# Optimization experiments

Measured on AMD Instinct MI355X. Metric: run time of the kernel, lower is better.

## Reference

```python
import jax, jax.numpy as jnp
import numpy as np

N = 100000   # num entities / tail rows
D_IN = 128
D_OUT = 128
R = 8        # num relations
E = 131072   # edges per relation
B = 32768    # head entities per relation


def setup_inputs() -> dict:
    key = jax.random.key(0)
    ks = jax.random.split(key, 8)
    x = jax.random.normal(ks[0], (N, D_IN), dtype=jnp.float32)
    tail_rep = jax.random.normal(ks[1], (N, D_IN), dtype=jnp.float32)
    # Linear(in, out, bias=False) weight: [out, in], xavier-ish scale
    W = jax.random.normal(ks[2], (D_OUT, D_IN), dtype=jnp.float32) * (1.414 / np.sqrt(D_IN))
    # match_matrix embedding -> per-relation [in, out] matrices
    rel_W = jax.random.normal(ks[3], (R, D_IN, D_OUT), dtype=jnp.float32) * (1.0 / np.sqrt(D_IN))
    edge_weights = jax.random.uniform(ks[4], (R, E), dtype=jnp.float32)
    edge_rows = jax.random.randint(ks[5], (R, E), 0, B, dtype=jnp.int32)
    edge_cols = jax.random.randint(ks[6], (R, E), 0, N, dtype=jnp.int32)
    # head_indice: unique global entity ids per relation (torch code assigns by index)
    rng = np.random.default_rng(0)
    head = np.stack([rng.choice(N, size=B, replace=False) for _ in range(R)]).astype(np.int32)
    head_indice = jnp.asarray(head)
    return {"x": x, "tail_rep": tail_rep, "W": W, "rel_W": rel_W,
            "edge_weights": edge_weights, "edge_rows": edge_rows,
            "edge_cols": edge_cols, "head_indice": head_indice}


def reference(x, tail_rep, W, rel_W, edge_weights, edge_rows, edge_cols, head_indice):
    # emb_all = original_map(input)
    emb_all = x @ W.T                                   # [N, D_OUT]
    # per-relation dense transform of all tails: tail_rep @ rel_W[r]
    transformed = jnp.einsum('ni,rio->rno', tail_rep, rel_W)   # [R, N, D_OUT]
    # sparse.mm(sp_edge_e, all_rep_h): gather tail rows per edge, weight, segment-sum by local head row
    gathered = jnp.take_along_axis(transformed, edge_cols[:, :, None], axis=1)  # [R, E, D_OUT]
    contrib = edge_weights[:, :, None] * gathered                                # [R, E, D_OUT]
    seg = lambda c, rows: jax.ops.segment_sum(c, rows, num_segments=B)
    new_rep = jax.vmap(seg)(contrib, edge_rows)                                  # [R, B, D_OUT]
    # emb_all[ent_indice] = rel_update + emb_all[ent_indice]  (per relation, sequentially) == scatter-add
    emb_all = emb_all.at[head_indice.reshape(-1)].add(new_rep.reshape(-1, D_OUT))
    # activate=True
    return jax.nn.relu(emb_all)
```

## Files before the change

kernel.cpp:

```cpp
#include <hip/hip_runtime.h>
#include <hip/hip_bf16.h>

#define D_DIM 128
#define N_ENT 100000
#define R_REL 8
#define E_EDGE 131072
#define B_HEAD 32768
#define NH_PAD 100352

typedef __attribute__((ext_vector_type(8))) short short8v;
typedef __attribute__((ext_vector_type(16))) float f32x16;
typedef unsigned int uint;
typedef unsigned short ushort;

union BF8 {
  short8v v;
  __hip_bfloat16 h[8];
};

__device__ inline ushort bfbits(float x) {
  union { __hip_bfloat16 h; ushort u; } c;
  c.h = __float2bfloat16(x);
  return c.u;
}
__device__ inline float bflo(uint p) { return __uint_as_float(p << 16); }
__device__ inline float bfhi(uint p) { return __uint_as_float(p & 0xffff0000u); }

__global__ __launch_bounds__(256) void init_ws(int* __restrict__ cnt_e,
                                               int* __restrict__ inv) {
  int i = blockIdx.x * 256 + threadIdx.x;
  if (i < R_REL * B_HEAD) cnt_e[i] = 0;
  inv[i] = -1;
}

__global__ __launch_bounds__(256) void prep_bf16(const float* __restrict__ src,
                                                 short8v* __restrict__ dst) {
  int i = blockIdx.x * 256 + threadIdx.x;
  const float4* s = (const float4*)src + (size_t)i * 2;
  float4 a = s[0], b = s[1];
  BF8 h;
  h.h[0] = __float2bfloat16(a.x); h.h[1] = __float2bfloat16(a.y);
  h.h[2] = __float2bfloat16(a.z); h.h[3] = __float2bfloat16(a.w);
  h.h[4] = __float2bfloat16(b.x); h.h[5] = __float2bfloat16(b.y);
  h.h[6] = __float2bfloat16(b.z); h.h[7] = __float2bfloat16(b.w);
  dst[i] = h.v;
}

__global__ __launch_bounds__(256) void hist_edges(const int* __restrict__ erow,
                                                  int* __restrict__ cnt) {
  int r = blockIdx.y;
  int e = blockIdx.x * 256 + threadIdx.x;
  int row = erow[(size_t)r * E_EDGE + e];
  atomicAdd(cnt + r * B_HEAD + row, 1);
}

__global__ __launch_bounds__(256) void scan_blk(const int* __restrict__ cnt,
                                                int* __restrict__ cur,
                                                int* __restrict__ bsum) {
  int b = blockIdx.x, t = threadIdx.x;
  int4 v = ((const int4*)cnt)[b * 256 + t];
  int s = v.x + v.y + v.z + v.w;
  __shared__ int ps[256];
  ps[t] = s;
  __syncthreads();
  for (int off = 1; off < 256; off <<= 1) {
    int u = (t >= off) ? ps[t - off] : 0;
    __syncthreads();
    ps[t] += u;
    __syncthreads();
  }
  int base = ps[t] - s;
  int4 o;
  o.x = base; o.y = base + v.x; o.z = o.y + v.y; o.w = o.z + v.z;
  ((int4*)cur)[b * 256 + t] = o;
  if (t == 255) bsum[b] = ps[255];
}

__global__ __launch_bounds__(256) void scan_bsum(int* __restrict__ bsum) {
  int t = threadIdx.x;
  int s = bsum[t];
  __shared__ int ps[256];
  ps[t] = s;
  __syncthreads();
  for (int off = 1; off < 256; off <<= 1) {
    int u = (t >= off) ? ps[t - off] : 0;
    __syncthreads();
    ps[t] += u;
    __syncthreads();
  }
  bsum[t] = ps[t] - s;
}

__global__ __launch_bounds__(256) void scan_add(int* __restrict__ cur,
                                                const int* __restrict__ bsum) {
  int i = blockIdx.x * 256 + threadIdx.x;
  int o = bsum[i >> 8];
  int4 v = ((int4*)cur)[i];
  v.x += o; v.y += o; v.z += o; v.w += o;
  ((int4*)cur)[i] = v;
}

__global__ __launch_bounds__(256) void scatter_edges(const int* __restrict__ erow,
                                                     const int* __restrict__ ecol,
                                                     const float* __restrict__ ew,
                                                     int* __restrict__ cur,
                                                     int2* __restrict__ sColW) {
  int r = blockIdx.y;
  int e = blockIdx.x * 256 + threadIdx.x;
  size_t idx = (size_t)r * E_EDGE + e;
  int row = erow[idx];
  int pos = atomicAdd(cur + r * B_HEAD + row, 1);
  sColW[pos] = make_int2(ecol[idx], __float_as_int(ew[idx]));
}

__global__ __launch_bounds__(256) void build_inv(const int* __restrict__ head,
                                                 int* __restrict__ inv) {
  int i = blockIdx.x * 256 + threadIdx.x;
  int r = i >> 15;
  inv[r * NH_PAD + head[i]] = i & (B_HEAD - 1);
}

__global__ __launch_bounds__(256) void csr_agg(const uint* __restrict__ tailb,
                                               const int* __restrict__ end_e,
                                               const int* __restrict__ cnt_e,
                                               const int2* __restrict__ sColW,
                                               uint* __restrict__ aggb, int r0) {
  int wid = (blockIdx.x << 2) + (threadIdx.x >> 6);
  int lane = threadIdx.x & 63;
  int f = r0 * B_HEAD + wid;
  int cn = cnt_e[f];
  int s = end_e[f] - cn;
  float ax = 0.f, ay = 0.f, bx = 0.f, by = 0.f;
  int k = 0;
  for (; k + 2 <= cn; k += 2) {
    int2 e0 = sColW[s + k];
    int2 e1 = sColW[s + k + 1];
    uint t0 = tailb[(size_t)e0.x * 64 + lane];
    uint t1 = tailb[(size_t)e1.x * 64 + lane];
    float w0 = __int_as_float(e0.y), w1 = __int_as_float(e1.y);
    ax += w0 * bflo(t0); ay += w0 * bfhi(t0);
    bx += w1 * bflo(t1); by += w1 * bfhi(t1);
  }
  if (k < cn) {
    int2 e0 = sColW[s + k];
    uint t0 = tailb[(size_t)e0.x * 64 + lane];
    float w0 = __int_as_float(e0.y);
    ax += w0 * bflo(t0); ay += w0 * bfhi(t0);
  }
  ax += bx; ay += by;
  aggb[(size_t)wid * 64 + lane] = (uint)bfbits(ax) | ((uint)bfbits(ay) << 16);
}

__global__ __launch_bounds__(256) void prep_W(const float* __restrict__ W,
                                              const float* __restrict__ relW,
                                              short8v* __restrict__ WhS,
                                              short8v* __restrict__ WlS) {
  int mat = blockIdx.y;
  int idx = blockIdx.x * 256 + threadIdx.x;
  int o = idx & 127, ks = idx >> 7;
  float v[8];
  if (mat == 0) {
    const float* src = W + o * D_DIM + ks * 8;
#pragma unroll
    for (int j = 0; j < 8; ++j) v[j] = src[j];
  } else {
    const float* src = relW + (size_t)(mat - 1) * D_DIM * D_DIM + (ks * 8) * D_DIM + o;
#pragma unroll
    for (int j = 0; j < 8; ++j) v[j] = src[j * D_DIM];
  }
  BF8 h, l;
#pragma unroll
  for (int j = 0; j < 8; ++j) {
    __hip_bfloat16 hb = __float2bfloat16(v[j]);
    h.h[j] = hb;
    l.h[j] = __float2bfloat16(v[j] - __bfloat162float(hb));
  }
  WhS[(size_t)mat * 2048 + idx] = h.v;
  WlS[(size_t)mat * 2048 + idx] = l.v;
}

__global__ __launch_bounds__(256) void gemm_all(const ushort* __restrict__ xb,
                                                const ushort* __restrict__ aggb,
                                                const short8v* __restrict__ WhS,
                                                const short8v* __restrict__ WlS,
                                                float* __restrict__ out,
                                                ushort* __restrict__ updb, int r0,
                                                int nxb) {
  __shared__ short8v wlds[2][8][128];
  int tid = threadIdx.x;
  int bid = blockIdx.x;
  bool xpart = (bid < nxb);
  const ushort* Abase;
  int mat, rowbase, relloc = 0;
  if (xpart) {
    Abase = xb;
    mat = 0;
    rowbase = bid * 128;
  } else {
    int b = bid - nxb;
    relloc = b >> 8;
    mat = 1 + r0 + relloc;
    rowbase = (b & 255) * 128;
    Abase = aggb + (size_t)relloc * B_HEAD * D_DIM;
  }
  const short8v* Hsrc = WhS + (size_t)mat * 2048;
  const short8v* Lsrc = WlS + (size_t)mat * 2048;
  int w = tid >> 6, lane = tid & 63, lrow = lane & 31, lsel = lane >> 5;
  int nrows = xpart ? N_ENT : B_HEAD;
  int arow = rowbase + w * 32 + lrow;
  int arowc = (arow < nrows) ? arow : (nrows - 1);
  const short8v* Arow = (const short8v*)(Abase + (size_t)arowc * D_DIM);

  f32x16 acc[4] = {};
  for (int half = 0; half < 2; ++half) {
    if (half) __syncthreads();
#pragma unroll
    for (int it = 0; it < 4; ++it) {
      int e = it * 256 + tid;
      wlds[0][e >> 7][e & 127] = Hsrc[half * 1024 + e];
      wlds[1][e >> 7][e & 127] = Lsrc[half * 1024 + e];
    }
    __syncthreads();
#pragma unroll
    for (int kk = 0; kk < 4; ++kk) {
      short8v a = Arow[half * 8 + kk * 2 + lsel];
      int ks = kk * 2 + lsel;
#pragma unroll
      for (int n = 0; n < 4; ++n) {
        short8v bh = wlds[0][ks][n * 32 + lrow];
        short8v bl = wlds[1][ks][n * 32 + lrow];
        acc[n] = __builtin_amdgcn_mfma_f32_32x32x16_bf16(a, bh, acc[n], 0, 0, 0);
        acc[n] = __builtin_amdgcn_mfma_f32_32x32x16_bf16(a, bl, acc[n], 0, 0, 0);
      }
    }
  }
  int wrow0 = rowbase + w * 32;
  if (xpart) {
#pragma unroll
    for (int reg = 0; reg < 16; ++reg) {
      int srow = wrow0 + (reg & 3) + 8 * (reg >> 2) + 4 * lsel;
      if (srow < N_ENT) {
        float* orow = out + (size_t)srow * D_DIM;
#pragma unroll
        for (int n = 0; n < 4; ++n) orow[n * 32 + lrow] = acc[n][reg];
      }
    }
  } else {
    ushort* ubase = updb + (size_t)relloc * B_HEAD * D_DIM;
#pragma unroll
    for (int reg = 0; reg < 16; ++reg) {
      int srow = wrow0 + (reg & 3) + 8 * (reg >> 2) + 4 * lsel;
      ushort* urow = ubase + (size_t)srow * D_DIM;
#pragma unroll
      for (int n = 0; n < 4; ++n) urow[n * 32 + lrow] = bfbits(acc[n][reg]);
    }
  }
}

__global__ __launch_bounds__(256) void final_add(const int* __restrict__ inv,
                                                 const ushort* __restrict__ updb,
                                                 float* __restrict__ out, int r0,
                                                 int c, int doRelu) {
  int n = blockIdx.x * 8 + (threadIdx.x >> 5);
  int lane = threadIdx.x & 31;
  if (n >= N_ENT) return;
  float4* o4 = (float4*)out + (size_t)n * 32 + lane;
  float4 v = *o4;
  for (int k = 0; k < c; ++k) {
    int row = inv[(r0 + k) * NH_PAD + n];
    if (row >= 0) {
      uint2 u = ((const uint2*)updb)[((size_t)k * B_HEAD + row) * 32 + lane];
      v.x += bflo(u.x); v.y += bfhi(u.x);
      v.z += bflo(u.y); v.w += bfhi(u.y);
    }
  }
  if (doRelu) {
    v.x = fmaxf(v.x, 0.f); v.y = fmaxf(v.y, 0.f);
    v.z = fmaxf(v.z, 0.f); v.w = fmaxf(v.w, 0.f);
  }
  *o4 = v;
}

extern "C" void kernel_launch(void* const* d_in, const int* in_sizes, int n_in,
                              void* d_out, int out_size, void* d_ws, size_t ws_size,
                              hipStream_t stream) {
  const float* x = (const float*)d_in[0];
  const float* tail = (const float*)d_in[1];
  const float* W = (const float*)d_in[2];
  const float* relW = (const float*)d_in[3];
  const float* ew = (const float*)d_in[4];
  const int* erow = (const int*)d_in[5];
  const int* ecol = (const int*)d_in[6];
  const int* head = (const int*)d_in[7];
  float* out = (float*)d_out;

  char* p = (char*)d_ws;
  short8v* WhS = (short8v*)p;   p += (size_t)(R_REL + 1) * 2048 * 16;
  short8v* WlS = (short8v*)p;   p += (size_t)(R_REL + 1) * 2048 * 16;
  short8v* tailb = (short8v*)p; p += (size_t)N_ENT * D_DIM * 2;
  short8v* xb = (short8v*)p;    p += (size_t)N_ENT * D_DIM * 2;
  int* cnt_e = (int*)p;         p += (size_t)R_REL * B_HEAD * 4;
  int* cur_e = (int*)p;         p += (size_t)R_REL * B_HEAD * 4;
  int* inv = (int*)p;           p += (size_t)R_REL * NH_PAD * 4;
  int* bsum = (int*)p;          p += 256 * 4;
  int2* sColW = (int2*)p;       p += (size_t)R_REL * E_EDGE * 8;
  char* dyn = p;
  size_t fixed = (size_t)(p - (char*)d_ws);
  size_t per_rel = (size_t)B_HEAD * D_DIM * 2 * 2;
  size_t avail = (ws_size > fixed) ? ws_size - fixed : 0;
  int chunk = (int)(avail / per_rel);
  if (chunk > R_REL) chunk = R_REL;
  if (chunk < 1) chunk = 1;
  ushort* aggb = (ushort*)dyn;
  ushort* updb = (ushort*)(dyn + (size_t)chunk * B_HEAD * D_DIM * 2);

  const int NXB = (N_ENT + 127) / 128;

  init_ws<<<dim3(R_REL * NH_PAD / 256), 256, 0, stream>>>(cnt_e, inv);
  prep_W<<<dim3(8, R_REL + 1), 256, 0, stream>>>(W, relW, WhS, WlS);
  prep_bf16<<<dim3(N_ENT * D_DIM / 8 / 256), 256, 0, stream>>>(tail, tailb);
  prep_bf16<<<dim3(N_ENT * D_DIM / 8 / 256), 256, 0, stream>>>(x, xb);

  hist_edges<<<dim3(E_EDGE / 256, R_REL), 256, 0, stream>>>(erow, cnt_e);
  scan_blk<<<dim3(256), 256, 0, stream>>>(cnt_e, cur_e, bsum);
  scan_bsum<<<dim3(1), 256, 0, stream>>>(bsum);
  scan_add<<<dim3(256), 256, 0, stream>>>(cur_e, bsum);
  scatter_edges<<<dim3(E_EDGE / 256, R_REL), 256, 0, stream>>>(erow, ecol, ew, cur_e,
                                                               sColW);
  build_inv<<<dim3(R_REL * B_HEAD / 256), 256, 0, stream>>>(head, inv);

  for (int r0 = 0; r0 < R_REL; r0 += chunk) {
    int c = (R_REL - r0 < chunk) ? (R_REL - r0) : chunk;
    csr_agg<<<dim3(c * B_HEAD / 4), 256, 0, stream>>>(
        (const uint*)tailb, cur_e, cnt_e, sColW, (uint*)aggb, r0);
    int nxb = (r0 == 0) ? NXB : 0;
    gemm_all<<<dim3(nxb + 256 * c), 256, 0, stream>>>(
        (const ushort*)xb, aggb, WhS, WlS, out, updb, r0, nxb);
    final_add<<<dim3((N_ENT + 7) / 8), 256, 0, stream>>>(inv, updb, out, r0, c,
                                                         (r0 + c == R_REL) ? 1 : 0);
  }
}
```

Before: 329.2 us.

## Merge small prep kernels and co-schedule x GEMM with CSR aggregation

Combines the two bf16 conversion launches into one, merges the edge histogram with the inverse-head build, and folds the scan offset add into the scatter and aggregation kernels so the scan_add launch is gone. The x@W GEMM blocks are interleaved with the CSR gather-aggregation blocks in a single launch, so compute-bound MFMA work overlaps with memory-bound gathers. The aggregation loop is also unrolled to four edges to keep more loads in flight. This cuts launch count and idle gaps between kernels, at the cost of heterogeneous blocks with shared LDS sizing and more complex indexing.

```diff
diff --git a/kernel.cpp b/kernel.cpp
--- a/kernel.cpp
+++ b/kernel.cpp
@@ -33,9 +33,20 @@
   inv[i] = -1;
 }
 
-__global__ __launch_bounds__(256) void prep_bf16(const float* __restrict__ src,
-                                                 short8v* __restrict__ dst) {
-  int i = blockIdx.x * 256 + threadIdx.x;
+__global__ __launch_bounds__(256) void prep_xt(const float* __restrict__ tail,
+                                               const float* __restrict__ x,
+                                               short8v* __restrict__ tailb,
+                                               short8v* __restrict__ xb) {
+  const int HALF = N_ENT * D_DIM / 8 / 256;
+  int bid = blockIdx.x;
+  const float* src;
+  short8v* dst;
+  int i;
+  if (bid < HALF) {
+    src = tail; dst = tailb; i = bid * 256 + threadIdx.x;
+  } else {
+    src = x; dst = xb; i = (bid - HALF) * 256 + threadIdx.x;
+  }
   const float4* s = (const float4*)src + (size_t)i * 2;
   float4 a = s[0], b = s[1];
   BF8 h;
@@ -46,12 +57,21 @@
   dst[i] = h.v;
 }
 
-__global__ __launch_bounds__(256) void hist_edges(const int* __restrict__ erow,
-                                                  int* __restrict__ cnt) {
-  int r = blockIdx.y;
-  int e = blockIdx.x * 256 + threadIdx.x;
-  int row = erow[(size_t)r * E_EDGE + e];
-  atomicAdd(cnt + r * B_HEAD + row, 1);
+__global__ __launch_bounds__(256) void hist_inv(const int* __restrict__ erow,
+                                                const int* __restrict__ head,
+                                                int* __restrict__ cnt,
+                                                int* __restrict__ inv) {
+  int bid = blockIdx.x;
+  if (bid < 4096) {
+    int r = bid >> 9;
+    int e = (bid & 511) * 256 + threadIdx.x;
+    int row = erow[(size_t)r * E_EDGE + e];
+    atomicAdd(cnt + r * B_HEAD + row, 1);
+  } else {
+    int i = (bid - 4096) * 256 + threadIdx.x;
+    int r = i >> 15;
+    inv[r * NH_PAD + head[i]] = i & (B_HEAD - 1);
+  }
 }
 
 __global__ __launch_bounds__(256) void scan_blk(const int* __restrict__ cnt,
@@ -91,64 +111,19 @@
   bsum[t] = ps[t] - s;
 }
 
-__global__ __launch_bounds__(256) void scan_add(int* __restrict__ cur,
-                                                const int* __restrict__ bsum) {
-  int i = blockIdx.x * 256 + threadIdx.x;
-  int o = bsum[i >> 8];
-  int4 v = ((int4*)cur)[i];
-  v.x += o; v.y += o; v.z += o; v.w += o;
-  ((int4*)cur)[i] = v;
-}
-
 __global__ __launch_bounds__(256) void scatter_edges(const int* __restrict__ erow,
                                                      const int* __restrict__ ecol,
                                                      const float* __restrict__ ew,
                                                      int* __restrict__ cur,
+                                                     const int* __restrict__ bsum,
                                                      int2* __restrict__ sColW) {
   int r = blockIdx.y;
   int e = blockIdx.x * 256 + threadIdx.x;
   size_t idx = (size_t)r * E_EDGE + e;
   int row = erow[idx];
-  int pos = atomicAdd(cur + r * B_HEAD + row, 1);
+  int gi = r * B_HEAD + row;
+  int pos = atomicAdd(cur + gi, 1) + bsum[gi >> 10];
   sColW[pos] = make_int2(ecol[idx], __float_as_int(ew[idx]));
-}
-
-__global__ __launch_bounds__(256) void build_inv(const int* __restrict__ head,
-                                                 int* __restrict__ inv) {
-  int i = blockIdx.x * 256 + threadIdx.x;
-  int r = i >> 15;
-  inv[r * NH_PAD + head[i]] = i & (B_HEAD - 1);
-}
-
-__global__ __launch_bounds__(256) void csr_agg(const uint* __restrict__ tailb,
-                                               const int* __restrict__ end_e,
-                                               const int* __restrict__ cnt_e,
-                                               const int2* __restrict__ sColW,
-                                               uint* __restrict__ aggb, int r0) {
-  int wid = (blockIdx.x << 2) + (threadIdx.x >> 6);
-  int lane = threadIdx.x & 63;
-  int f = r0 * B_HEAD + wid;
-  int cn = cnt_e[f];
-  int s = end_e[f] - cn;
-  float ax = 0.f, ay = 0.f, bx = 0.f, by = 0.f;
-  int k = 0;
-  for (; k + 2 <= cn; k += 2) {
-    int2 e0 = sColW[s + k];
-    int2 e1 = sColW[s + k + 1];
-    uint t0 = tailb[(size_t)e0.x * 64 + lane];
-    uint t1 = tailb[(size_t)e1.x * 64 + lane];
-    float w0 = __int_as_float(e0.y), w1 = __int_as_float(e1.y);
-    ax += w0 * bflo(t0); ay += w0 * bfhi(t0);
-    bx += w1 * bflo(t1); by += w1 * bfhi(t1);
-  }
-  if (k < cn) {
-    int2 e0 = sColW[s + k];
-    uint t0 = tailb[(size_t)e0.x * 64 + lane];
-    float w0 = __int_as_float(e0.y);
-    ax += w0 * bflo(t0); ay += w0 * bfhi(t0);
-  }
-  ax += bx; ay += by;
-  aggb[(size_t)wid * 64 + lane] = (uint)bfbits(ax) | ((uint)bfbits(ay) << 16);
 }
 
 __global__ __launch_bounds__(256) void prep_W(const float* __restrict__ W,
@@ -179,37 +154,111 @@
   WlS[(size_t)mat * 2048 + idx] = l.v;
 }
 
-__global__ __launch_bounds__(256) void gemm_all(const ushort* __restrict__ xb,
-                                                const ushort* __restrict__ aggb,
+__global__ __launch_bounds__(256) void fused_agg_gemmx(
+    const uint* __restrict__ tailb, const ushort* __restrict__ xb,
+    const short8v* __restrict__ WhS, const short8v* __restrict__ WlS,
+    int* __restrict__ cur_e, const int* __restrict__ cnt_e,
+    const int* __restrict__ bsum, const int2* __restrict__ sColW,
+    uint* __restrict__ aggb, float* __restrict__ out, int r0, int nxb, int P,
+    int csrB) {
+  __shared__ short8v wlds[2][8][128];
+  int bid = blockIdx.x;
+  int tid = threadIdx.x;
+  bool isg = (nxb > 0) && (bid % P == 0);
+
+  if (isg) {
+    int gid = bid / P;
+    int w = tid >> 6, lane = tid & 63, lrow = lane & 31, lsel = lane >> 5;
+    int rowbase = gid * 128;
+    int arow = rowbase + w * 32 + lrow;
+    int arowc = (arow < N_ENT) ? arow : (N_ENT - 1);
+    const short8v* Arow = (const short8v*)(xb + (size_t)arowc * D_DIM);
+    f32x16 acc[4] = {};
+    for (int half = 0; half < 2; ++half) {
+      if (half) __syncthreads();
+#pragma unroll
+      for (int it = 0; it < 4; ++it) {
+        int e = it * 256 + tid;
+        wlds[0][e >> 7][e & 127] = WhS[half * 1024 + e];
+        wlds[1][e >> 7][e & 127] = WlS[half * 1024 + e];
+      }
+      __syncthreads();
+#pragma unroll
+      for (int kk = 0; kk < 4; ++kk) {
+        short8v a = Arow[half * 8 + kk * 2 + lsel];
+        int ks = kk * 2 + lsel;
+#pragma unroll
+        for (int n = 0; n < 4; ++n) {
+          short8v bh = wlds[0][ks][n * 32 + lrow];
+          short8v bl = wlds[1][ks][n * 32 + lrow];
+          acc[n] = __builtin_amdgcn_mfma_f32_32x32x16_bf16(a, bh, acc[n], 0, 0, 0);
+          acc[n] = __builtin_amdgcn_mfma_f32_32x32x16_bf16(a, bl, acc[n], 0, 0, 0);
+        }
+      }
+    }
+    int wrow0 = rowbase + w * 32;
+#pragma unroll
+    for (int reg = 0; reg < 16; ++reg) {
+      int srow = wrow0 + (reg & 3) + 8 * (reg >> 2) + 4 * lsel;
+      if (srow < N_ENT) {
+        float* orow = out + (size_t)srow * D_DIM;
+#pragma unroll
+        for (int n = 0; n < 4; ++n) orow[n * 32 + lrow] = acc[n][reg];
+      }
+    }
+    return;
+  }
+
+  int cid = (nxb > 0) ? (bid - bid / P - 1) : bid;
+  if (cid >= csrB) return;
+  int wid = (cid << 2) + (tid >> 6);
+  int lane = tid & 63;
+  int f = r0 * B_HEAD + wid;
+  int cn = cnt_e[f];
+  int s = cur_e[f] - cn + bsum[f >> 10];
+  float a0x = 0.f, a0y = 0.f, a1x = 0.f, a1y = 0.f;
+  float a2x = 0.f, a2y = 0.f, a3x = 0.f, a3y = 0.f;
+  int k = 0;
+  for (; k + 4 <= cn; k += 4) {
+    int2 e0 = sColW[s + k], e1 = sColW[s + k + 1];
+    int2 e2 = sColW[s + k + 2], e3 = sColW[s + k + 3];
+    uint t0 = tailb[(size_t)e0.x * 64 + lane];
+    uint t1 = tailb[(size_t)e1.x * 64 + lane];
+    uint t2 = tailb[(size_t)e2.x * 64 + lane];
+    uint t3 = tailb[(size_t)e3.x * 64 + lane];
+    float w0 = __int_as_float(e0.y), w1 = __int_as_float(e1.y);
+    float w2 = __int_as_float(e2.y), w3 = __int_as_float(e3.y);
+    a0x += w0 * bflo(t0); a0y += w0 * bfhi(t0);
+    a1x += w1 * bflo(t1); a1y += w1 * bfhi(t1);
+    a2x += w2 * bflo(t2); a2y += w2 * bfhi(t2);
+    a3x += w3 * bflo(t3); a3y += w3 * bfhi(t3);
+  }
+  for (; k < cn; ++k) {
+    int2 e0 = sColW[s + k];
+    uint t0 = tailb[(size_t)e0.x * 64 + lane];
+    float w0 = __int_as_float(e0.y);
+    a0x += w0 * bflo(t0); a0y += w0 * bfhi(t0);
+  }
+  a0x += a1x + a2x + a3x;
+  a0y += a1y + a2y + a3y;
+  aggb[(size_t)wid * 64 + lane] = (uint)bfbits(a0x) | ((uint)bfbits(a0y) << 16);
+}
+
+__global__ __launch_bounds__(256) void gemm_rel(const ushort* __restrict__ aggb,
                                                 const short8v* __restrict__ WhS,
                                                 const short8v* __restrict__ WlS,
-                                                float* __restrict__ out,
-                                                ushort* __restrict__ updb, int r0,
-                                                int nxb) {
+                                                ushort* __restrict__ updb, int r0) {
   __shared__ short8v wlds[2][8][128];
   int tid = threadIdx.x;
-  int bid = blockIdx.x;
-  bool xpart = (bid < nxb);
-  const ushort* Abase;
-  int mat, rowbase, relloc = 0;
-  if (xpart) {
-    Abase = xb;
-    mat = 0;
-    rowbase = bid * 128;
-  } else {
-    int b = bid - nxb;
-    relloc = b >> 8;
-    mat = 1 + r0 + relloc;
-    rowbase = (b & 255) * 128;
-    Abase = aggb + (size_t)relloc * B_HEAD * D_DIM;
-  }
+  int relloc = blockIdx.y;
+  int mat = 1 + r0 + relloc;
   const short8v* Hsrc = WhS + (size_t)mat * 2048;
   const short8v* Lsrc = WlS + (size_t)mat * 2048;
   int w = tid >> 6, lane = tid & 63, lrow = lane & 31, lsel = lane >> 5;
-  int nrows = xpart ? N_ENT : B_HEAD;
+  int rowbase = blockIdx.x * 128;
   int arow = rowbase + w * 32 + lrow;
-  int arowc = (arow < nrows) ? arow : (nrows - 1);
-  const short8v* Arow = (const short8v*)(Abase + (size_t)arowc * D_DIM);
+  const short8v* Arow =
+      (const short8v*)(aggb + ((size_t)relloc * B_HEAD + arow) * D_DIM);
 
   f32x16 acc[4] = {};
   for (int half = 0; half < 2; ++half) {
@@ -235,25 +284,13 @@
     }
   }
   int wrow0 = rowbase + w * 32;
-  if (xpart) {
-#pragma unroll
-    for (int reg = 0; reg < 16; ++reg) {
-      int srow = wrow0 + (reg & 3) + 8 * (reg >> 2) + 4 * lsel;
-      if (srow < N_ENT) {
-        float* orow = out + (size_t)srow * D_DIM;
-#pragma unroll
-        for (int n = 0; n < 4; ++n) orow[n * 32 + lrow] = acc[n][reg];
-      }
-    }
-  } else {
-    ushort* ubase = updb + (size_t)relloc * B_HEAD * D_DIM;
-#pragma unroll
-    for (int reg = 0; reg < 16; ++reg) {
-      int srow = wrow0 + (reg & 3) + 8 * (reg >> 2) + 4 * lsel;
-      ushort* urow = ubase + (size_t)srow * D_DIM;
-#pragma unroll
-      for (int n = 0; n < 4; ++n) urow[n * 32 + lrow] = bfbits(acc[n][reg]);
-    }
+  ushort* ubase = updb + (size_t)relloc * B_HEAD * D_DIM;
+#pragma unroll
+  for (int reg = 0; reg < 16; ++reg) {
+    int srow = wrow0 + (reg & 3) + 8 * (reg >> 2) + 4 * lsel;
+    ushort* urow = ubase + (size_t)srow * D_DIM;
+#pragma unroll
+    for (int n = 0; n < 4; ++n) urow[n * 32 + lrow] = bfbits(acc[n][reg]);
   }
 }
 
@@ -318,24 +355,28 @@
 
   init_ws<<<dim3(R_REL * NH_PAD / 256), 256, 0, stream>>>(cnt_e, inv);
   prep_W<<<dim3(8, R_REL + 1), 256, 0, stream>>>(W, relW, WhS, WlS);
-  prep_bf16<<<dim3(N_ENT * D_DIM / 8 / 256), 256, 0, stream>>>(tail, tailb);
-  prep_bf16<<<dim3(N_ENT * D_DIM / 8 / 256), 256, 0, stream>>>(x, xb);
-
-  hist_edges<<<dim3(E_EDGE / 256, R_REL), 256, 0, stream>>>(erow, cnt_e);
+  prep_xt<<<dim3(2 * (N_ENT * D_DIM / 8 / 256)), 256, 0, stream>>>(tail, x, tailb, xb);
+
+  hist_inv<<<dim3(4096 + R_REL * B_HEAD / 256), 256, 0, stream>>>(erow, head, cnt_e,
+                                                                  inv);
   scan_blk<<<dim3(256), 256, 0, stream>>>(cnt_e, cur_e, bsum);
   scan_bsum<<<dim3(1), 256, 0, stream>>>(bsum);
-  scan_add<<<dim3(256), 256, 0, stream>>>(cur_e, bsum);
   scatter_edges<<<dim3(E_EDGE / 256, R_REL), 256, 0, stream>>>(erow, ecol, ew, cur_e,
-                                                               sColW);
-  build_inv<<<dim3(R_REL * B_HEAD / 256), 256, 0, stream>>>(head, inv);
+                                                               bsum, sColW);
 
   for (int r0 = 0; r0 < R_REL; r0 += chunk) {
     int c = (R_REL - r0 < chunk) ? (R_REL - r0) : chunk;
-    csr_agg<<<dim3(c * B_HEAD / 4), 256, 0, stream>>>(
-        (const uint*)tailb, cur_e, cnt_e, sColW, (uint*)aggb, r0);
+    int csrB = c * B_HEAD / 4;
     int nxb = (r0 == 0) ? NXB : 0;
-    gemm_all<<<dim3(nxb + 256 * c), 256, 0, stream>>>(
-        (const ushort*)xb, aggb, WhS, WlS, out, updb, r0, nxb);
+    int P = 1, grid = csrB;
+    if (nxb > 0) {
+      P = (csrB + nxb - 1) / nxb + 1;
+      grid = nxb * P;
+    }
+    fused_agg_gemmx<<<dim3(grid), 256, 0, stream>>>(
+        (const uint*)tailb, (const ushort*)xb, WhS, WlS, cur_e, cnt_e, bsum, sColW,
+        (uint*)aggb, out, r0, nxb, P, csrB);
+    gemm_rel<<<dim3(B_HEAD / 128, c), 256, 0, stream>>>(aggb, WhS, WlS, updb, r0);
     final_add<<<dim3((N_ENT + 7) / 8), 256, 0, stream>>>(inv, updb, out, r0, c,
                                                          (r0 + c == R_REL) ? 1 : 0);
   }
```

Result: slower. 445.4 us (+35.3%).

## Merge prep kernels, fold scan offset into consumers, batch edge loads in aggregation

Applied to the files above, without the earlier changes.

Merges the two bf16 conversion launches into one, and merges the histogram with the inverse-index build. It also drops the scan_add pass by adding the block prefix offset directly in scatter_edges and csr_agg. csr_agg now handles two head rows per wavefront and loads eight edge records cooperatively, broadcasting them with shuffles so more tail-row gathers are in flight at once. The goal is fewer kernel launches and better latency hiding in the gather; the cost is extra shuffles and predicated work when the two rows have unequal edge counts.

```diff
diff --git a/kernel.cpp b/kernel.cpp
--- a/kernel.cpp
+++ b/kernel.cpp
@@ -7,6 +7,7 @@
 #define E_EDGE 131072
 #define B_HEAD 32768
 #define NH_PAD 100352
+#define MAXE (R_REL * E_EDGE)
 
 typedef __attribute__((ext_vector_type(8))) short short8v;
 typedef __attribute__((ext_vector_type(16))) float f32x16;
@@ -33,9 +34,20 @@
   inv[i] = -1;
 }
 
-__global__ __launch_bounds__(256) void prep_bf16(const float* __restrict__ src,
-                                                 short8v* __restrict__ dst) {
-  int i = blockIdx.x * 256 + threadIdx.x;
+__global__ __launch_bounds__(256) void prep_xt(const float* __restrict__ tail,
+                                               const float* __restrict__ x,
+                                               short8v* __restrict__ tailb,
+                                               short8v* __restrict__ xb) {
+  const int HALF = N_ENT * D_DIM / 8 / 256;
+  int bid = blockIdx.x;
+  const float* src;
+  short8v* dst;
+  int i;
+  if (bid < HALF) {
+    src = tail; dst = tailb; i = bid * 256 + threadIdx.x;
+  } else {
+    src = x; dst = xb; i = (bid - HALF) * 256 + threadIdx.x;
+  }
   const float4* s = (const float4*)src + (size_t)i * 2;
   float4 a = s[0], b = s[1];
   BF8 h;
@@ -46,12 +58,21 @@
   dst[i] = h.v;
 }
 
-__global__ __launch_bounds__(256) void hist_edges(const int* __restrict__ erow,
-                                                  int* __restrict__ cnt) {
-  int r = blockIdx.y;
-  int e = blockIdx.x * 256 + threadIdx.x;
-  int row = erow[(size_t)r * E_EDGE + e];
-  atomicAdd(cnt + r * B_HEAD + row, 1);
+__global__ __launch_bounds__(256) void hist_inv(const int* __restrict__ erow,
+                                                const int* __restrict__ head,
+                                                int* __restrict__ cnt,
+                                                int* __restrict__ inv) {
+  int bid = blockIdx.x;
+  if (bid < 4096) {
+    int r = bid >> 9;
+    int e = (bid & 511) * 256 + threadIdx.x;
+    int row = erow[(size_t)r * E_EDGE + e];
+    atomicAdd(cnt + r * B_HEAD + row, 1);
+  } else {
+    int i = (bid - 4096) * 256 + threadIdx.x;
+    int r = i >> 15;
+    inv[r * NH_PAD + head[i]] = i & (B_HEAD - 1);
+  }
 }
 
 __global__ __launch_bounds__(256) void scan_blk(const int* __restrict__ cnt,
@@ -91,64 +112,19 @@
   bsum[t] = ps[t] - s;
 }
 
-__global__ __launch_bounds__(256) void scan_add(int* __restrict__ cur,
-                                                const int* __restrict__ bsum) {
-  int i = blockIdx.x * 256 + threadIdx.x;
-  int o = bsum[i >> 8];
-  int4 v = ((int4*)cur)[i];
-  v.x += o; v.y += o; v.z += o; v.w += o;
-  ((int4*)cur)[i] = v;
-}
-
 __global__ __launch_bounds__(256) void scatter_edges(const int* __restrict__ erow,
                                                      const int* __restrict__ ecol,
                                                      const float* __restrict__ ew,
                                                      int* __restrict__ cur,
+                                                     const int* __restrict__ bsum,
                                                      int2* __restrict__ sColW) {
   int r = blockIdx.y;
   int e = blockIdx.x * 256 + threadIdx.x;
   size_t idx = (size_t)r * E_EDGE + e;
   int row = erow[idx];
-  int pos = atomicAdd(cur + r * B_HEAD + row, 1);
+  int gi = r * B_HEAD + row;
+  int pos = atomicAdd(cur + gi, 1) + bsum[gi >> 10];
   sColW[pos] = make_int2(ecol[idx], __float_as_int(ew[idx]));
-}
-
-__global__ __launch_bounds__(256) void build_inv(const int* __restrict__ head,
-                                                 int* __restrict__ inv) {
-  int i = blockIdx.x * 256 + threadIdx.x;
-  int r = i >> 15;
-  inv[r * NH_PAD + head[i]] = i & (B_HEAD - 1);
-}
-
-__global__ __launch_bounds__(256) void csr_agg(const uint* __restrict__ tailb,
-                                               const int* __restrict__ end_e,
-                                               const int* __restrict__ cnt_e,
-                                               const int2* __restrict__ sColW,
-                                               uint* __restrict__ aggb, int r0) {
-  int wid = (blockIdx.x << 2) + (threadIdx.x >> 6);
-  int lane = threadIdx.x & 63;
-  int f = r0 * B_HEAD + wid;
-  int cn = cnt_e[f];
-  int s = end_e[f] - cn;
-  float ax = 0.f, ay = 0.f, bx = 0.f, by = 0.f;
-  int k = 0;
-  for (; k + 2 <= cn; k += 2) {
-    int2 e0 = sColW[s + k];
-    int2 e1 = sColW[s + k + 1];
-    uint t0 = tailb[(size_t)e0.x * 64 + lane];
-    uint t1 = tailb[(size_t)e1.x * 64 + lane];
-    float w0 = __int_as_float(e0.y), w1 = __int_as_float(e1.y);
-    ax += w0 * bflo(t0); ay += w0 * bfhi(t0);
-    bx += w1 * bflo(t1); by += w1 * bfhi(t1);
-  }
-  if (k < cn) {
-    int2 e0 = sColW[s + k];
-    uint t0 = tailb[(size_t)e0.x * 64 + lane];
-    float w0 = __int_as_float(e0.y);
-    ax += w0 * bflo(t0); ay += w0 * bfhi(t0);
-  }
-  ax += bx; ay += by;
-  aggb[(size_t)wid * 64 + lane] = (uint)bfbits(ax) | ((uint)bfbits(ay) << 16);
 }
 
 __global__ __launch_bounds__(256) void prep_W(const float* __restrict__ W,
@@ -177,6 +153,49 @@
   }
   WhS[(size_t)mat * 2048 + idx] = h.v;
   WlS[(size_t)mat * 2048 + idx] = l.v;
+}
+
+__global__ __launch_bounds__(256) void csr_agg(const uint* __restrict__ tailb,
+                                               const int* __restrict__ cur_e,
+                                               const int* __restrict__ cnt_e,
+                                               const int* __restrict__ bsum,
+                                               const int2* __restrict__ sColW,
+                                               uint* __restrict__ aggb, int r0) {
+  int base = (blockIdx.x << 3) + ((threadIdx.x >> 6) << 1);
+  int lane = threadIdx.x & 63;
+  int li = lane & 7;
+  int f0 = r0 * B_HEAD + base, f1 = f0 + 1;
+  int cn0 = cnt_e[f0], cn1 = cnt_e[f1];
+  int s0 = cur_e[f0] - cn0 + bsum[f0 >> 10];
+  int s1 = cur_e[f1] - cn1 + bsum[f1 >> 10];
+  float a0x = 0.f, a0y = 0.f, a1x = 0.f, a1y = 0.f;
+  int rounds = ((cn0 > cn1 ? cn0 : cn1) + 7) >> 3;
+  for (int rr = 0; rr < rounds; ++rr) {
+    int k = rr << 3;
+    int i0 = k + li; if (i0 > cn0 - 1) i0 = cn0 > 0 ? cn0 - 1 : 0;
+    int i1 = k + li; if (i1 > cn1 - 1) i1 = cn1 > 0 ? cn1 - 1 : 0;
+    int g0 = s0 + i0; if (g0 > MAXE - 1) g0 = MAXE - 1;
+    int g1 = s1 + i1; if (g1 > MAXE - 1) g1 = MAXE - 1;
+    int2 ea = sColW[g0];
+    int2 eb = sColW[g1];
+#pragma unroll
+    for (int j = 0; j < 8; ++j) {
+      if (k + j < cn0) {
+        int col = __shfl(ea.x, j, 8);
+        float w = __int_as_float(__shfl(ea.y, j, 8));
+        uint t = tailb[(size_t)col * 64 + lane];
+        a0x += w * bflo(t); a0y += w * bfhi(t);
+      }
+      if (k + j < cn1) {
+        int col = __shfl(eb.x, j, 8);
+        float w = __int_as_float(__shfl(eb.y, j, 8));
+        uint t = tailb[(size_t)col * 64 + lane];
+        a1x += w * bflo(t); a1y += w * bfhi(t);
+      }
+    }
+  }
+  aggb[(size_t)base * 64 + lane] = (uint)bfbits(a0x) | ((uint)bfbits(a0y) << 16);
+  aggb[(size_t)(base + 1) * 64 + lane] = (uint)bfbits(a1x) | ((uint)bfbits(a1y) << 16);
 }
 
 __global__ __launch_bounds__(256) void gemm_all(const ushort* __restrict__ xb,
@@ -318,21 +337,19 @@
 
   init_ws<<<dim3(R_REL * NH_PAD / 256), 256, 0, stream>>>(cnt_e, inv);
   prep_W<<<dim3(8, R_REL + 1), 256, 0, stream>>>(W, relW, WhS, WlS);
-  prep_bf16<<<dim3(N_ENT * D_DIM / 8 / 256), 256, 0, stream>>>(tail, tailb);
-  prep_bf16<<<dim3(N_ENT * D_DIM / 8 / 256), 256, 0, stream>>>(x, xb);
-
-  hist_edges<<<dim3(E_EDGE / 256, R_REL), 256, 0, stream>>>(erow, cnt_e);
+  prep_xt<<<dim3(2 * (N_ENT * D_DIM / 8 / 256)), 256, 0, stream>>>(tail, x, tailb, xb);
+
+  hist_inv<<<dim3(4096 + R_REL * B_HEAD / 256), 256, 0, stream>>>(erow, head, cnt_e,
+                                                                  inv);
   scan_blk<<<dim3(256), 256, 0, stream>>>(cnt_e, cur_e, bsum);
   scan_bsum<<<dim3(1), 256, 0, stream>>>(bsum);
-  scan_add<<<dim3(256), 256, 0, stream>>>(cur_e, bsum);
   scatter_edges<<<dim3(E_EDGE / 256, R_REL), 256, 0, stream>>>(erow, ecol, ew, cur_e,
-                                                               sColW);
-  build_inv<<<dim3(R_REL * B_HEAD / 256), 256, 0, stream>>>(head, inv);
+                                                               bsum, sColW);
 
   for (int r0 = 0; r0 < R_REL; r0 += chunk) {
     int c = (R_REL - r0 < chunk) ? (R_REL - r0) : chunk;
-    csr_agg<<<dim3(c * B_HEAD / 4), 256, 0, stream>>>(
-        (const uint*)tailb, cur_e, cnt_e, sColW, (uint*)aggb, r0);
+    csr_agg<<<dim3(c * B_HEAD / 8), 256, 0, stream>>>(
+        (const uint*)tailb, cur_e, cnt_e, bsum, sColW, (uint*)aggb, r0);
     int nxb = (r0 == 0) ? NXB : 0;
     gemm_all<<<dim3(nxb + 256 * c), 256, 0, stream>>>(
         (const ushort*)xb, aggb, WhS, WlS, out, updb, r0, nxb);
```

Measured after the change: 329.6 us. Within noise of the previous version (+0.1%).
